# Kernel tuning notes

Measured on AMD Instinct MI355X. Metric: run time of the kernel, lower is better.

## Reference

```python
import jax, jax.numpy as jnp
import numpy as np

N = 10000        # num_nodes
D = 256          # num_attrs
AVG_DEG = 32
K = N // 2       # known nodes
ALPHA = 0.5
BETA = 0.5


def setup_inputs() -> dict:
    rng = np.random.default_rng(0)
    # random graph -> symmetric adjacency (duplicate edges coalesce by summation,
    # matching torch_geometric coalescing of edge weights)
    src = rng.integers(0, N, size=N * AVG_DEG)
    dst = rng.integers(0, N, size=N * AVG_DEG)
    A = np.zeros((N, N), dtype=np.float32)
    np.add.at(A, (src, dst), 1.0)
    np.add.at(A, (dst, src), 1.0)
    # symmetric normalized Laplacian: L = I - D^{-1/2} A D^{-1/2}
    deg = A.sum(axis=1)
    dinv = np.where(deg > 0, 1.0 / np.sqrt(np.maximum(deg, 1e-12)), 0.0).astype(np.float32)
    L = np.eye(N, dtype=np.float32) - (dinv[:, None] * A * dinv[None, :])

    raw_x = rng.standard_normal((N, D)).astype(np.float32)
    know = np.sort(rng.choice(N, size=K, replace=False)).astype(np.int64)
    mean = raw_x[know].mean(axis=0)                 # is_binary=False path
    out_k_init = (raw_x[know] - mean).astype(np.float32)  # std = 1
    x = np.zeros((N, D), dtype=np.float32)
    x[know] = raw_x[know]                           # nn.Parameter init

    theta = np.float32((1.0 - 1.0 / N) * (1.0 / ALPHA - 1.0))
    eta = np.float32((1.0 / BETA - 1.0) / ALPHA)
    return {
        "x": jnp.asarray(x),
        "L": jnp.asarray(L),
        "mean": jnp.asarray(mean),
        "out_k_init": jnp.asarray(out_k_init),
        "know_mask": jnp.asarray(know),
        "theta": jnp.asarray(theta),
        "eta": jnp.asarray(eta),
    }


def reference(x, L, mean, out_k_init, know_mask, theta, eta):
    n = x.shape[0]
    xn = x - mean  # std = 1
    # dirichlet loss: sum_f x_f^T L x_f == sum(xn * (L @ xn))
    dirichlet = jnp.sum(xn * (L @ xn))
    # avg_L = n/(n-1) I - 1/(n-1) 11^T  ->  quadratic form in closed form
    col = xn.sum(axis=0)  # [D]
    avg = (n / (n - 1)) * jnp.sum(xn * xn) - (1.0 / (n - 1)) * jnp.sum(col * col)
    # MSE with reduction='sum'
    recon = jnp.sum((xn[know_mask] - out_k_init) ** 2)
    return -(dirichlet + eta * recon + theta * avg)
```

## Files before the change

### kernel.cpp

```cpp
#include <hip/hip_runtime.h>


#define NN    10000
#define DD    256
#define PREPB 157
#define SBLK  1250
#define QCAP  2048

typedef float  f32x4 __attribute__((ext_vector_type(4)));
typedef short  s16x8 __attribute__((ext_vector_type(8)));

__device__ __forceinline__ unsigned short f2bf(float f) {
    union { float f; unsigned u; } c; c.f = f;
    unsigned u = c.u;
    u += 0x7fffu + ((u >> 16) & 1u);
    return (unsigned short)(u >> 16);
}
__device__ __forceinline__ float bfr(unsigned short h) {
    union { unsigned u; float f; } c; c.u = ((unsigned)h) << 16; return c.f;
}

__global__ __launch_bounds__(256) void prep_kernel(const float* __restrict__ x,
                                                   const float* __restrict__ mean,
                                                   unsigned short* __restrict__ xnR,
                                                   float* __restrict__ csbuf,
                                                   float* __restrict__ ssbuf) {
    __shared__ __align__(16) unsigned short xs[64][264];
    __shared__ float red[4];
    const int t  = threadIdx.x;
    const int i0 = blockIdx.x * 64;
    const float mn = mean[t];
    float css = 0.f, ss = 0.f;
    for (int ii = 0; ii < 64; ++ii) {
        const int i = i0 + ii;
        float v = 0.f;
        if (i < NN) v = x[(size_t)i * DD + t] - mn;
        css += v; ss += v * v;
        xs[ii][t] = f2bf(v);
    }
    csbuf[(size_t)blockIdx.x * 256 + t] = css;
#pragma unroll
    for (int off = 32; off > 0; off >>= 1) ss += __shfl_xor(ss, off);
    if ((t & 63) == 0) red[t >> 6] = ss;
    __syncthreads();
    if (t == 0) ssbuf[blockIdx.x] = red[0] + red[1] + red[2] + red[3];
#pragma unroll
    for (int p = 0; p < 8; ++p) {
        const int row  = p * 8 + (t >> 5);
        const int colb = (t & 31) * 8;
        const int i = i0 + row;
        if (i < NN)
            *(s16x8*)(xnR + (size_t)i * DD + colb) = *(const s16x8*)&xs[row][colb];
    }
}

__global__ __launch_bounds__(256) void recon_kernel(const float* __restrict__ x,
                                                    const float* __restrict__ mean,
                                                    const float* __restrict__ oki,
                                                    const int* __restrict__ know,
                                                    int K, float* __restrict__ rbuf) {
    __shared__ float red[4];
    const int t = threadIdx.x;
    const float mn = mean[t];
    float s = 0.f;
    for (int b = blockIdx.x; b < K; b += gridDim.x) {
        const int idx = know[b];
        const float v = x[(size_t)idx * DD + t] - mn - oki[(size_t)b * DD + t];
        s += v * v;
    }
#pragma unroll
    for (int off = 32; off > 0; off >>= 1) s += __shfl_xor(s, off);
    if ((t & 63) == 0) red[t >> 6] = s;
    __syncthreads();
    if (t == 0) rbuf[blockIdx.x] = red[0] + red[1] + red[2] + red[3];
}

__global__ __launch_bounds__(256) void sdot_kernel(const float* __restrict__ L,
                                                   const unsigned short* __restrict__ xnR,
                                                   float* __restrict__ part) {
    __shared__ unsigned qidx[QCAP];
    __shared__ float    qval[QCAP];
    __shared__ unsigned qcnt;
    __shared__ float red[4];
    const int t = threadIdx.x;
    const int b = blockIdx.x;
    if (t == 0) qcnt = 0;
    __syncthreads();

    const int ibt = 4 * b;
    const int ibb = NN - 8 - 4 * b;
#define ROWLEN(i_) ((NN - (((i_) >> 2) << 2) + 15) >> 4)
    const int l0 = ROWLEN(ibt);     const int l1 = ROWLEN(ibt + 1);
    const int l2 = ROWLEN(ibt + 2); const int l3 = ROWLEN(ibt + 3);
    const int l4 = ROWLEN(ibb + 4); const int l5 = ROWLEN(ibb + 5);
    const int l6 = ROWLEN(ibb + 6);
    const int pre1 = l0;        const int pre2 = pre1 + l1;
    const int pre3 = pre2 + l2; const int pre4 = pre3 + l3;
    const int pre5 = pre4 + l4; const int pre6 = pre5 + l5;
    const int pre7 = pre6 + l6;
    const int ntot = pre7 + ROWLEN(ibb + 7);
#undef ROWLEN

#define DECODE(g_)                                                             \
    int rr_ = 0, base_ = 0;                                                    \
    if ((g_) >= pre1) { rr_ = 1; base_ = pre1; }                               \
    if ((g_) >= pre2) { rr_ = 2; base_ = pre2; }                               \
    if ((g_) >= pre3) { rr_ = 3; base_ = pre3; }                               \
    if ((g_) >= pre4) { rr_ = 4; base_ = pre4; }                               \
    if ((g_) >= pre5) { rr_ = 5; base_ = pre5; }                               \
    if ((g_) >= pre6) { rr_ = 6; base_ = pre6; }                               \
    if ((g_) >= pre7) { rr_ = 7; base_ = pre7; }                               \
    const int i_ = (rr_ < 4) ? (ibt + rr_) : (ibb + rr_);                      \
    const int c_ = (((i_) >> 2) << 2) + (((g_) - base_) << 4);

#define ISSUE(V0_, V1_, V2_, V3_, g_) {                                        \
    if ((g_) < ntot) {                                                         \
        DECODE(g_)                                                             \
        const float* p_ = L + (size_t)i_ * NN + c_;                            \
        if (c_ + 16 <= NN) {                                                   \
            V0_ = *(const f32x4*)p_;        V1_ = *(const f32x4*)(p_ + 4);     \
            V2_ = *(const f32x4*)(p_ + 8);  V3_ = *(const f32x4*)(p_ + 12);    \
        } else {                                                               \
            _Pragma("unroll") for (int e_ = 0; e_ < 4; ++e_) {                 \
                V0_[e_] = (c_ + e_      < NN) ? p_[e_]      : 0.f;             \
                V1_[e_] = (c_ + e_ + 4  < NN) ? p_[e_ + 4]  : 0.f;             \
                V2_[e_] = (c_ + e_ + 8  < NN) ? p_[e_ + 8]  : 0.f;             \
                V3_[e_] = (c_ + e_ + 12 < NN) ? p_[e_ + 12] : 0.f;             \
            } } } }

#define PROC(V0_, V1_, V2_, V3_, g_) {                                         \
    if ((g_) < ntot) {                                                         \
        DECODE(g_)                                                             \
        _Pragma("unroll") for (int e_ = 0; e_ < 16; ++e_) {                    \
            const float v_ = (e_ < 4) ? V0_[e_] : (e_ < 8) ? V1_[e_ - 4]       \
                           : (e_ < 12) ? V2_[e_ - 8] : V3_[e_ - 12];           \
            const int j_ = c_ + e_;                                            \
            if (v_ != 0.f && j_ >= i_ && j_ < NN) {                            \
                const unsigned s_ = atomicAdd(&qcnt, 1u);                      \
                if (s_ < QCAP) {                                               \
                    qidx[s_] = ((unsigned)rr_ << 14) | (unsigned)j_;           \
                    qval[s_] = (j_ == i_) ? v_ : 2.f * v_;                     \
                } } } } }

    f32x4 A0, A1, A2, A3, B0, B1, B2, B3, C0, C1, C2, C3;
    int g = t;
    ISSUE(A0, A1, A2, A3, g)
    ISSUE(B0, B1, B2, B3, g + 256)
    ISSUE(C0, C1, C2, C3, g + 512)
    while (g < ntot) {
        PROC (A0, A1, A2, A3, g)
        ISSUE(A0, A1, A2, A3, g + 768)
        PROC (B0, B1, B2, B3, g + 256)
        ISSUE(B0, B1, B2, B3, g + 1024)
        PROC (C0, C1, C2, C3, g + 512)
        ISSUE(C0, C1, C2, C3, g + 1280)
        g += 768;
    }
#undef ISSUE
#undef PROC
#undef DECODE
    __syncthreads();
    const unsigned cnt = (qcnt < QCAP) ? qcnt : QCAP;

    const int grp = t >> 4;
    const int ln  = t & 15;
    float acc = 0.f;
    for (unsigned e = grp; e < cnt; e += 32) {
        const unsigned e2   = e + 16;
        const bool     has2 = (e2 < cnt);
        const unsigned pkA = qidx[e];
        const unsigned pkB = has2 ? qidx[e2] : pkA;
        const int rrA = (int)(pkA >> 14), jA = (int)(pkA & 16383u);
        const int rrB = (int)(pkB >> 14), jB = (int)(pkB & 16383u);
        const int iA  = (rrA < 4) ? (ibt + rrA) : (ibb + rrA);
        const int iB  = (rrB < 4) ? (ibt + rrB) : (ibb + rrB);
        const unsigned short* riA = xnR + (size_t)iA * DD + ln * 16;
        const unsigned short* rjA = xnR + (size_t)jA * DD + ln * 16;
        const unsigned short* riB = xnR + (size_t)iB * DD + ln * 16;
        const unsigned short* rjB = xnR + (size_t)jB * DD + ln * 16;
        const s16x8 a0 = *(const s16x8*)riA, a1 = *(const s16x8*)(riA + 8);
        const s16x8 b0 = *(const s16x8*)rjA, b1 = *(const s16x8*)(rjA + 8);
        const s16x8 c0 = *(const s16x8*)riB, c1 = *(const s16x8*)(riB + 8);
        const s16x8 d0 = *(const s16x8*)rjB, d1 = *(const s16x8*)(rjB + 8);
        float dA = 0.f, dB = 0.f;
#pragma unroll
        for (int k = 0; k < 8; ++k) {
            dA += bfr((unsigned short)a0[k]) * bfr((unsigned short)b0[k]);
            dB += bfr((unsigned short)c0[k]) * bfr((unsigned short)d0[k]);
        }
#pragma unroll
        for (int k = 0; k < 8; ++k) {
            dA += bfr((unsigned short)a1[k]) * bfr((unsigned short)b1[k]);
            dB += bfr((unsigned short)c1[k]) * bfr((unsigned short)d1[k]);
        }
#pragma unroll
        for (int off = 1; off < 16; off <<= 1) {
            dA += __shfl_xor(dA, off);
            dB += __shfl_xor(dB, off);
        }
        if (ln == 0) {
            acc += qval[e] * dA;
            if (has2) acc += qval[e2] * dB;
        }
    }
#pragma unroll
    for (int off = 32; off > 0; off >>= 1) acc += __shfl_xor(acc, off);
    if ((t & 63) == 0) red[t >> 6] = acc;
    __syncthreads();
    if (t == 0) part[b] = red[0] + red[1] + red[2] + red[3];
}

__global__ __launch_bounds__(256) void fin_kernel(const float* __restrict__ part,
                                                  const float* __restrict__ csbuf,
                                                  const float* __restrict__ ssbuf,
                                                  const float* __restrict__ rbuf,
                                                  const float* __restrict__ theta,
                                                  const float* __restrict__ eta,
                                                  float* __restrict__ out) {
    __shared__ float red[4][4];
    const int t = threadIdx.x;
    float sp = 0.f;
    for (int i = t; i < SBLK; i += 256) sp += part[i];
    float cs = 0.f;
    for (int bb = 0; bb < PREPB; ++bb) cs += csbuf[(size_t)bb * 256 + t];
    float c2 = cs * cs;
    float ssv = (t < PREPB) ? ssbuf[t] : 0.f;
    float rv  = rbuf[t];
#pragma unroll
    for (int off = 32; off > 0; off >>= 1) {
        sp  += __shfl_xor(sp, off);
        c2  += __shfl_xor(c2, off);
        ssv += __shfl_xor(ssv, off);
        rv  += __shfl_xor(rv, off);
    }
    if ((t & 63) == 0) {
        red[t >> 6][0] = sp; red[t >> 6][1] = c2;
        red[t >> 6][2] = ssv; red[t >> 6][3] = rv;
    }
    __syncthreads();
    if (t == 0) {
        float dir = 0.f, colsq = 0.f, ss = 0.f, rec = 0.f;
#pragma unroll
        for (int w = 0; w < 4; ++w) {
            dir += red[w][0]; colsq += red[w][1];
            ss  += red[w][2]; rec   += red[w][3];
        }
        const float n = (float)NN;
        const float avg = (n / (n - 1.f)) * ss - colsq / (n - 1.f);
        out[0] = -(dir + eta[0] * rec + theta[0] * avg);
    }
}

extern "C" void kernel_launch(void* const* d_in, const int* in_sizes, int n_in,
                              void* d_out, int out_size, void* d_ws, size_t ws_size,
                              hipStream_t stream) {
    const float* x     = (const float*)d_in[0];
    const float* L     = (const float*)d_in[1];
    const float* mean  = (const float*)d_in[2];
    const float* oki   = (const float*)d_in[3];
    const int*   know  = (const int*)d_in[4];
    const float* theta = (const float*)d_in[5];
    const float* eta   = (const float*)d_in[6];
    float* out = (float*)d_out;

    char* ws = (char*)d_ws;
    unsigned short* xnR = (unsigned short*)ws;
    float* part  = (float*)(ws + 6 * 1024 * 1024);
    float* csbuf = (float*)(ws + 7 * 1024 * 1024);
    float* ssbuf = (float*)(ws + 8 * 1024 * 1024);
    float* rbuf  = (float*)(ws + 8 * 1024 * 1024 + 4096);
    const int K = in_sizes[4];

    hipLaunchKernelGGL(prep_kernel,  dim3(PREPB), dim3(256), 0, stream, x, mean, xnR, csbuf, ssbuf);
    hipLaunchKernelGGL(recon_kernel, dim3(256),   dim3(256), 0, stream, x, mean, oki, know, K, rbuf);
    hipLaunchKernelGGL(sdot_kernel,  dim3(SBLK),  dim3(256), 0, stream, L, xnR, part);
    hipLaunchKernelGGL(fin_kernel,   dim3(1),     dim3(256), 0, stream, part, csbuf, ssbuf, rbuf, theta, eta, out);
}
```

Before: 101.8 us.

## Fuse recon into prep kernel, vectorize loads, cache i-rows in LDS for sdot

Merges the reconstruction-loss kernel into the prep kernel as extra blocks, removing one launch and letting the two run concurrently. Both paths now use float4 loads, and prep computes the column sums from the bf16 tile in LDS. In sdot, the 8 row vectors each block uses are staged in shared memory, and the dot-product phase now uses 8-lane groups that each cover 32 elements, which reduces global reloads of the i-rows and the shuffle steps. Column sums are now taken from bf16-rounded values, which slightly changes numerics, and the extra LDS may reduce occupancy.

```diff
diff --git a/kernel.cpp b/kernel.cpp
--- a/kernel.cpp
+++ b/kernel.cpp
@@ -4,11 +4,13 @@
 #define NN    10000
 #define DD    256
 #define PREPB 157
+#define RECB  256
 #define SBLK  1250
 #define QCAP  2048
 
 typedef float  f32x4 __attribute__((ext_vector_type(4)));
 typedef short  s16x8 __attribute__((ext_vector_type(8)));
+typedef short  s16x4 __attribute__((ext_vector_type(4)));
 
 __device__ __forceinline__ unsigned short f2bf(float f) {
     union { float f; unsigned u; } c; c.f = f;
@@ -22,57 +24,75 @@
 
 __global__ __launch_bounds__(256) void prep_kernel(const float* __restrict__ x,
                                                    const float* __restrict__ mean,
+                                                   const float* __restrict__ oki,
+                                                   const int* __restrict__ know,
+                                                   int K,
                                                    unsigned short* __restrict__ xnR,
                                                    float* __restrict__ csbuf,
-                                                   float* __restrict__ ssbuf) {
+                                                   float* __restrict__ ssbuf,
+                                                   float* __restrict__ rbuf) {
     __shared__ __align__(16) unsigned short xs[64][264];
-    __shared__ float red[4];
+    __shared__ float red[8];
     const int t  = threadIdx.x;
-    const int i0 = blockIdx.x * 64;
-    const float mn = mean[t];
-    float css = 0.f, ss = 0.f;
-    for (int ii = 0; ii < 64; ++ii) {
-        const int i = i0 + ii;
-        float v = 0.f;
-        if (i < NN) v = x[(size_t)i * DD + t] - mn;
-        css += v; ss += v * v;
-        xs[ii][t] = f2bf(v);
-    }
-    csbuf[(size_t)blockIdx.x * 256 + t] = css;
-#pragma unroll
-    for (int off = 32; off > 0; off >>= 1) ss += __shfl_xor(ss, off);
-    if ((t & 63) == 0) red[t >> 6] = ss;
-    __syncthreads();
-    if (t == 0) ssbuf[blockIdx.x] = red[0] + red[1] + red[2] + red[3];
-#pragma unroll
-    for (int p = 0; p < 8; ++p) {
-        const int row  = p * 8 + (t >> 5);
-        const int colb = (t & 31) * 8;
-        const int i = i0 + row;
-        if (i < NN)
-            *(s16x8*)(xnR + (size_t)i * DD + colb) = *(const s16x8*)&xs[row][colb];
-    }
-}
-
-__global__ __launch_bounds__(256) void recon_kernel(const float* __restrict__ x,
-                                                    const float* __restrict__ mean,
-                                                    const float* __restrict__ oki,
-                                                    const int* __restrict__ know,
-                                                    int K, float* __restrict__ rbuf) {
-    __shared__ float red[4];
-    const int t = threadIdx.x;
-    const float mn = mean[t];
-    float s = 0.f;
-    for (int b = blockIdx.x; b < K; b += gridDim.x) {
-        const int idx = know[b];
-        const float v = x[(size_t)idx * DD + t] - mn - oki[(size_t)b * DD + t];
-        s += v * v;
-    }
-#pragma unroll
-    for (int off = 32; off > 0; off >>= 1) s += __shfl_xor(s, off);
-    if ((t & 63) == 0) red[t >> 6] = s;
-    __syncthreads();
-    if (t == 0) rbuf[blockIdx.x] = red[0] + red[1] + red[2] + red[3];
+    const int bb = blockIdx.x;
+    if (bb < PREPB) {
+        const int i0 = bb * 64;
+        float ss = 0.f;
+#pragma unroll
+        for (int p = 0; p < 16; ++p) {
+            const int li  = p * 256 + t;
+            const int row = li >> 6;
+            const int c4  = li & 63;
+            const int gi  = i0 + row;
+            f32x4 v = {0.f, 0.f, 0.f, 0.f};
+            if (gi < NN) {
+                const f32x4 xv = *(const f32x4*)(x + (size_t)gi * DD + c4 * 4);
+                const f32x4 mv = *(const f32x4*)(mean + c4 * 4);
+                v[0] = xv[0] - mv[0]; v[1] = xv[1] - mv[1];
+                v[2] = xv[2] - mv[2]; v[3] = xv[3] - mv[3];
+                ss += v[0]*v[0] + v[1]*v[1] + v[2]*v[2] + v[3]*v[3];
+            }
+            unsigned short h[4];
+            h[0] = f2bf(v[0]); h[1] = f2bf(v[1]); h[2] = f2bf(v[2]); h[3] = f2bf(v[3]);
+            *(s16x4*)&xs[row][c4 * 4] = *(const s16x4*)h;
+        }
+#pragma unroll
+        for (int off = 32; off > 0; off >>= 1) ss += __shfl_xor(ss, off);
+        if ((t & 63) == 0) red[t >> 6] = ss;
+        __syncthreads();
+        if (t == 0) ssbuf[bb] = red[0] + red[1] + red[2] + red[3];
+        float css = 0.f;
+        for (int ii = 0; ii < 64; ++ii) css += bfr(xs[ii][t]);
+        csbuf[(size_t)bb * 256 + t] = css;
+#pragma unroll
+        for (int p = 0; p < 8; ++p) {
+            const int row  = p * 8 + (t >> 5);
+            const int colb = (t & 31) * 8;
+            const int i = i0 + row;
+            if (i < NN)
+                *(s16x8*)(xnR + (size_t)i * DD + colb) = *(const s16x8*)&xs[row][colb];
+        }
+    } else {
+        const int rb = bb - PREPB;
+        const int w  = t >> 6, l = t & 63;
+        const f32x4 mv = *(const f32x4*)(mean + l * 4);
+        float s = 0.f;
+        for (int r = rb * 4 + w; r < K; r += RECB * 4) {
+            const int idx = know[r];
+            const f32x4 xv = *(const f32x4*)(x   + (size_t)idx * DD + l * 4);
+            const f32x4 ov = *(const f32x4*)(oki + (size_t)r   * DD + l * 4);
+            const float d0 = xv[0] - mv[0] - ov[0];
+            const float d1 = xv[1] - mv[1] - ov[1];
+            const float d2 = xv[2] - mv[2] - ov[2];
+            const float d3 = xv[3] - mv[3] - ov[3];
+            s += d0*d0 + d1*d1 + d2*d2 + d3*d3;
+        }
+#pragma unroll
+        for (int off = 32; off > 0; off >>= 1) s += __shfl_xor(s, off);
+        if (l == 0) red[4 + w] = s;
+        __syncthreads();
+        if (t == 0) rbuf[rb] = red[4] + red[5] + red[6] + red[7];
+    }
 }
 
 __global__ __launch_bounds__(256) void sdot_kernel(const float* __restrict__ L,
@@ -80,15 +100,21 @@
                                                    float* __restrict__ part) {
     __shared__ unsigned qidx[QCAP];
     __shared__ float    qval[QCAP];
+    __shared__ __align__(16) unsigned short irw[8][264];
     __shared__ unsigned qcnt;
     __shared__ float red[4];
     const int t = threadIdx.x;
     const int b = blockIdx.x;
-    if (t == 0) qcnt = 0;
-    __syncthreads();
-
     const int ibt = 4 * b;
     const int ibb = NN - 8 - 4 * b;
+    if (t == 0) qcnt = 0;
+    {
+        const int sr = t >> 5, sc = (t & 31) * 8;
+        const int si = (sr < 4) ? (ibt + sr) : (ibb + sr);
+        *(s16x8*)&irw[sr][sc] = *(const s16x8*)(xnR + (size_t)si * DD + sc);
+    }
+    __syncthreads();
+
 #define ROWLEN(i_) ((NN - (((i_) >> 2) << 2) + 15) >> 4)
     const int l0 = ROWLEN(ibt);     const int l1 = ROWLEN(ibt + 1);
     const int l2 = ROWLEN(ibt + 2); const int l3 = ROWLEN(ibt + 3);
@@ -162,45 +188,64 @@
     __syncthreads();
     const unsigned cnt = (qcnt < QCAP) ? qcnt : QCAP;
 
-    const int grp = t >> 4;
-    const int ln  = t & 15;
+    const int grp = t >> 3;
+    const int ln  = t & 7;
+    const int cb  = ln * 32;
     float acc = 0.f;
-    for (unsigned e = grp; e < cnt; e += 32) {
-        const unsigned e2   = e + 16;
-        const bool     has2 = (e2 < cnt);
+    for (unsigned e = grp; e < cnt; e += 64) {
+        const unsigned eB  = e + 32;
+        const bool     hasB = (eB < cnt);
         const unsigned pkA = qidx[e];
-        const unsigned pkB = has2 ? qidx[e2] : pkA;
+        const unsigned pkB = hasB ? qidx[eB] : pkA;
         const int rrA = (int)(pkA >> 14), jA = (int)(pkA & 16383u);
         const int rrB = (int)(pkB >> 14), jB = (int)(pkB & 16383u);
-        const int iA  = (rrA < 4) ? (ibt + rrA) : (ibb + rrA);
-        const int iB  = (rrB < 4) ? (ibt + rrB) : (ibb + rrB);
-        const unsigned short* riA = xnR + (size_t)iA * DD + ln * 16;
-        const unsigned short* rjA = xnR + (size_t)jA * DD + ln * 16;
-        const unsigned short* riB = xnR + (size_t)iB * DD + ln * 16;
-        const unsigned short* rjB = xnR + (size_t)jB * DD + ln * 16;
-        const s16x8 a0 = *(const s16x8*)riA, a1 = *(const s16x8*)(riA + 8);
-        const s16x8 b0 = *(const s16x8*)rjA, b1 = *(const s16x8*)(rjA + 8);
-        const s16x8 c0 = *(const s16x8*)riB, c1 = *(const s16x8*)(riB + 8);
-        const s16x8 d0 = *(const s16x8*)rjB, d1 = *(const s16x8*)(rjB + 8);
+        const unsigned short* pjA = xnR + (size_t)jA * DD + cb;
+        const unsigned short* pjB = xnR + (size_t)jB * DD + cb;
         float dA = 0.f, dB = 0.f;
-#pragma unroll
-        for (int k = 0; k < 8; ++k) {
-            dA += bfr((unsigned short)a0[k]) * bfr((unsigned short)b0[k]);
-            dB += bfr((unsigned short)c0[k]) * bfr((unsigned short)d0[k]);
-        }
-#pragma unroll
-        for (int k = 0; k < 8; ++k) {
-            dA += bfr((unsigned short)a1[k]) * bfr((unsigned short)b1[k]);
-            dB += bfr((unsigned short)c1[k]) * bfr((unsigned short)d1[k]);
-        }
-#pragma unroll
-        for (int off = 1; off < 16; off <<= 1) {
+        {
+            const s16x8 ja0 = *(const s16x8*)pjA,       ja1 = *(const s16x8*)(pjA + 8);
+            const s16x8 jb0 = *(const s16x8*)pjB,       jb1 = *(const s16x8*)(pjB + 8);
+            const s16x8 ia0 = *(const s16x8*)&irw[rrA][cb];
+            const s16x8 ia1 = *(const s16x8*)&irw[rrA][cb + 8];
+            const s16x8 ib0 = *(const s16x8*)&irw[rrB][cb];
+            const s16x8 ib1 = *(const s16x8*)&irw[rrB][cb + 8];
+#pragma unroll
+            for (int k = 0; k < 8; ++k) {
+                dA += bfr((unsigned short)ia0[k]) * bfr((unsigned short)ja0[k]);
+                dB += bfr((unsigned short)ib0[k]) * bfr((unsigned short)jb0[k]);
+            }
+#pragma unroll
+            for (int k = 0; k < 8; ++k) {
+                dA += bfr((unsigned short)ia1[k]) * bfr((unsigned short)ja1[k]);
+                dB += bfr((unsigned short)ib1[k]) * bfr((unsigned short)jb1[k]);
+            }
+        }
+        {
+            const s16x8 ja2 = *(const s16x8*)(pjA + 16), ja3 = *(const s16x8*)(pjA + 24);
+            const s16x8 jb2 = *(const s16x8*)(pjB + 16), jb3 = *(const s16x8*)(pjB + 24);
+            const s16x8 ia2 = *(const s16x8*)&irw[rrA][cb + 16];
+            const s16x8 ia3 = *(const s16x8*)&irw[rrA][cb + 24];
+            const s16x8 ib2 = *(const s16x8*)&irw[rrB][cb + 16];
+            const s16x8 ib3 = *(const s16x8*)&irw[rrB][cb + 24];
+#pragma unroll
+            for (int k = 0; k < 8; ++k) {
+                dA += bfr((unsigned short)ia2[k]) * bfr((unsigned short)ja2[k]);
+                dB += bfr((unsigned short)ib2[k]) * bfr((unsigned short)jb2[k]);
+            }
+#pragma unroll
+            for (int k = 0; k < 8; ++k) {
+                dA += bfr((unsigned short)ia3[k]) * bfr((unsigned short)ja3[k]);
+                dB += bfr((unsigned short)ib3[k]) * bfr((unsigned short)jb3[k]);
+            }
+        }
+#pragma unroll
+        for (int off = 1; off < 8; off <<= 1) {
             dA += __shfl_xor(dA, off);
             dB += __shfl_xor(dB, off);
         }
         if (ln == 0) {
             acc += qval[e] * dA;
-            if (has2) acc += qval[e2] * dB;
+            if (hasB) acc += qval[eB] * dB;
         }
     }
 #pragma unroll
@@ -271,8 +316,9 @@
     float* rbuf  = (float*)(ws + 8 * 1024 * 1024 + 4096);
     const int K = in_sizes[4];
 
-    hipLaunchKernelGGL(prep_kernel,  dim3(PREPB), dim3(256), 0, stream, x, mean, xnR, csbuf, ssbuf);
-    hipLaunchKernelGGL(recon_kernel, dim3(256),   dim3(256), 0, stream, x, mean, oki, know, K, rbuf);
-    hipLaunchKernelGGL(sdot_kernel,  dim3(SBLK),  dim3(256), 0, stream, L, xnR, part);
-    hipLaunchKernelGGL(fin_kernel,   dim3(1),     dim3(256), 0, stream, part, csbuf, ssbuf, rbuf, theta, eta, out);
-}
+    hipLaunchKernelGGL(prep_kernel, dim3(PREPB + RECB), dim3(256), 0, stream,
+                       x, mean, oki, know, K, xnR, csbuf, ssbuf, rbuf);
+    hipLaunchKernelGGL(sdot_kernel, dim3(SBLK), dim3(256), 0, stream, L, xnR, part);
+    hipLaunchKernelGGL(fin_kernel,  dim3(1),    dim3(256), 0, stream,
+                       part, csbuf, ssbuf, rbuf, theta, eta, out);
+}
```

Measured after the change: 81.80 us (median of 2 runs). 19.7% less time.
